# Optimization experiments

Measured on AMD Instinct MI355X. Metric: run time of the kernel, lower is better.

The kernel has to match this reference:

```python
import jax, jax.numpy as jnp
import numpy as np

B, T, D = 2, 512, 1024
H = 16
DH = D // H          # 64 head dim
E = 8                # experts
K = 2                # top-k routing
F = 4 * D            # expert hidden dim


def _layernorm(x, s, b, eps=1e-5):
    mu = jnp.mean(x, axis=-1, keepdims=True)
    var = jnp.var(x, axis=-1, keepdims=True)
    return (x - mu) * jax.lax.rsqrt(var + eps) * s + b


def setup_inputs() -> dict:
    key = jax.random.key(0)
    ks = jax.random.split(key, 16)
    sd = 0.02
    return {
        "x": jax.random.normal(ks[0], (B, T, D), jnp.float32),
        "text_state": jax.random.normal(ks[1], (B, D), jnp.float32),
        "ln1_s": jnp.ones((D,), jnp.float32),
        "ln1_b": jnp.zeros((D,), jnp.float32),
        "w_qkv": jax.random.normal(ks[2], (D, 3 * D), jnp.float32) * sd,
        "b_qkv": jnp.zeros((3 * D,), jnp.float32),
        "w_o": jax.random.normal(ks[3], (D, D), jnp.float32) * sd,
        "b_o": jnp.zeros((D,), jnp.float32),
        "rel_bias": jax.random.normal(ks[4], (H, 2 * T - 1), jnp.float32) * sd,
        "ln2_s": jnp.ones((D,), jnp.float32),
        "ln2_b": jnp.zeros((D,), jnp.float32),
        "w_txt": jax.random.normal(ks[5], (D, D), jnp.float32) * sd,
        "b_txt": jnp.zeros((D,), jnp.float32),
        "w_r": jax.random.normal(ks[6], (D, E), jnp.float32) * sd,
        "b_r": jnp.zeros((E,), jnp.float32),
        "w1": jax.random.normal(ks[7], (E, D, F), jnp.float32) * sd,
        "b1": jnp.zeros((E, F), jnp.float32),
        "w2": jax.random.normal(ks[8], (E, F, D), jnp.float32) * sd,
        "b2": jnp.zeros((E, D), jnp.float32),
    }


def reference(x, text_state, ln1_s, ln1_b, w_qkv, b_qkv, w_o, b_o, rel_bias,
              ln2_s, ln2_b, w_txt, b_txt, w_r, b_r, w1, b1, w2, b2):
    # ---- temporal-bias multi-head self-attention (pre-LN, residual) ----
    h = _layernorm(x, ln1_s, ln1_b)
    qkv = (h @ w_qkv + b_qkv).reshape(B, T, 3, H, DH)
    q, k, v = qkv[:, :, 0], qkv[:, :, 1], qkv[:, :, 2]       # [B,T,H,DH]
    scores = jnp.einsum("bthd,bshd->bhts", q, k) / np.sqrt(DH).astype(np.float32)
    idx = jnp.arange(T)
    rel = idx[None, :] - idx[:, None] + (T - 1)              # [T,T] in [0, 2T-2]
    scores = scores + rel_bias[:, rel][None]                 # broadcast [1,H,T,T]
    attn = jax.nn.softmax(scores, axis=-1)
    ctx = jnp.einsum("bhts,bshd->bthd", attn, v).reshape(B, T, D)
    x = x + ctx @ w_o + b_o

    # ---- top-k MoE feed-forward with text-conditioned router ----
    h2 = _layernorm(x, ln2_s, ln2_b)
    router_in = h2 + (text_state @ w_txt + b_txt)[:, None, :]
    probs = jax.nn.softmax(router_in @ w_r + b_r, axis=-1)   # [B,T,E]
    topv, topi = jax.lax.top_k(probs, K)                     # [B,T,K]
    gates = topv / jnp.sum(topv, axis=-1, keepdims=True)
    gates_full = jnp.einsum("btk,btke->bte", gates, jax.nn.one_hot(topi, E, dtype=x.dtype))
    # dense grouped-expert compute, sparsely combined (same math as dispatch)
    hid = jax.nn.gelu(jnp.einsum("btd,edf->btef", h2, w1) + b1)      # [B,T,E,F]
    eout = jnp.einsum("btef,efd->bted", hid, w2) + b2                # [B,T,E,D]
    y = jnp.einsum("bte,bted->btd", gates_full, eout)
    x = x + y

    diag = jnp.mean(probs, axis=(0, 1))                      # expert load [E]
    return x, diag
```

## Files before the change

kernel.cpp:

```cpp
#include <hip/hip_runtime.h>
#include <hip/hip_bf16.h>
#include <math.h>

#define BB 2
#define TT 512
#define DD 1024
#define HH 16
#define DHH 64
#define EE 8
#define FF 4096
#define NTOK 1024
#define CAP 2560
#define SPL 2

typedef __attribute__((ext_vector_type(4))) float f32x4;
typedef __attribute__((ext_vector_type(8))) short short8;

__device__ __forceinline__ short f2b(float f) {
    __hip_bfloat16 h = __float2bfloat16(f);
    return *reinterpret_cast<short*>(&h);
}
__device__ __forceinline__ float b2f(short s) {
    __hip_bfloat16 h = *reinterpret_cast<__hip_bfloat16*>(&s);
    return __bfloat162float(h);
}

__device__ __forceinline__ void gload16(const short* g, short* l) {
    __builtin_amdgcn_global_load_lds((const __attribute__((address_space(1))) unsigned int*)g,
                                     (__attribute__((address_space(3))) unsigned int*)l,
                                     16, 0, 0);
}

template <int BF>
__global__ __launch_bounds__(256) void ln_kernel(const float* __restrict__ x,
                                                 const float* __restrict__ s,
                                                 const float* __restrict__ b,
                                                 void* __restrict__ outp) {
    int row = blockIdx.x;
    int tid = threadIdx.x;
    const float* xr = x + (size_t)row * DD;
    float sm = 0.f, sq = 0.f;
    for (int i = tid; i < DD; i += 256) {
        float v = xr[i];
        sm += v; sq += v * v;
    }
    #pragma unroll
    for (int o = 32; o; o >>= 1) {
        sm += __shfl_down(sm, o);
        sq += __shfl_down(sq, o);
    }
    __shared__ float r1[4], r2[4];
    if ((tid & 63) == 0) { r1[tid >> 6] = sm; r2[tid >> 6] = sq; }
    __syncthreads();
    float tot  = r1[0] + r1[1] + r1[2] + r1[3];
    float totq = r2[0] + r2[1] + r2[2] + r2[3];
    float mu  = tot * (1.f / DD);
    float var = totq * (1.f / DD) - mu * mu;
    float inv = rsqrtf(var + 1e-5f);
    for (int i = tid; i < DD; i += 256) {
        float v = (xr[i] - mu) * inv * s[i] + b[i];
        if (BF) ((short*)outp)[(size_t)row * DD + i] = f2b(v);
        else    ((float*)outp)[(size_t)row * DD + i] = v;
    }
}

__global__ __launch_bounds__(256) void transpose_cast(const float* __restrict__ src,
                                                      short* __restrict__ dst,
                                                      int K, int N) {
    __shared__ float t[64][65];
    src += (size_t)blockIdx.z * K * N;
    dst += (size_t)blockIdx.z * K * N;
    int k0 = blockIdx.y * 64, n0 = blockIdx.x * 64;
    int rr = threadIdx.x >> 4;
    int cc = (threadIdx.x & 15) * 4;
    #pragma unroll
    for (int p = 0; p < 4; p++) {
        float4 v = *(const float4*)&src[(size_t)(k0 + rr + p * 16) * N + n0 + cc];
        t[rr + p * 16][cc]     = v.x;
        t[rr + p * 16][cc + 1] = v.y;
        t[rr + p * 16][cc + 2] = v.z;
        t[rr + p * 16][cc + 3] = v.w;
    }
    __syncthreads();
    #pragma unroll
    for (int p = 0; p < 4; p++) {
        int n = rr + p * 16;
        short4 o;
        o.x = f2b(t[cc][n]); o.y = f2b(t[cc + 1][n]);
        o.z = f2b(t[cc + 2][n]); o.w = f2b(t[cc + 3][n]);
        *(short4*)&dst[(size_t)(n0 + n) * K + k0 + cc] = o;
    }
}

__global__ __launch_bounds__(256) void v_transpose(const short* __restrict__ Vb,
                                                   short* __restrict__ VTb) {
    __shared__ short t[32][33];
    int bh = blockIdx.z;
    const short* src = Vb + (size_t)bh * TT * DHH;
    short* dst = VTb + (size_t)bh * DHH * TT;
    int t0 = blockIdx.x * 32, d0 = blockIdx.y * 32;
    int tx = threadIdx.x & 31, ty = threadIdx.x >> 5;
    #pragma unroll
    for (int p = 0; p < 4; p++)
        t[ty + p * 8][tx] = src[(size_t)(t0 + ty + p * 8) * DHH + d0 + tx];
    __syncthreads();
    #pragma unroll
    for (int p = 0; p < 4; p++)
        dst[(size_t)(d0 + ty + p * 8) * TT + t0 + tx] = t[tx][ty + p * 8];
}

__device__ __forceinline__ void gemm_loop64(const short* __restrict__ A,
                                            const short* __restrict__ B,
                                            int K, int lda, int ldb,
                                            short* As, short* Bs,
                                            f32x4 acc[2][2], int m0, int n0, int tid) {
    int wave = tid >> 6, lane = tid & 63;
    int wr = wave >> 1, wc = wave & 1;
    int lrow = lane & 15, lk = lane >> 4;
    int sr = tid >> 3, ss = tid & 7;
    int sswz = (ss ^ (sr & 7)) * 8;
    const short* Ag0 = A + (size_t)(m0 + sr) * lda + sswz;
    const short* Ag1 = A + (size_t)(m0 + sr + 32) * lda + sswz;
    const short* Bg0 = B + (size_t)(n0 + sr) * ldb + sswz;
    const short* Bg1 = B + (size_t)(n0 + sr + 32) * ldb + sswz;
    short* lA0 = As + wave * 512;
    short* lA1 = As + 2048 + wave * 512;
    short* lB0 = Bs + wave * 512;
    short* lB1 = Bs + 2048 + wave * 512;
    int nt = K >> 6;
    gload16(Ag0, lA0); gload16(Ag1, lA1);
    gload16(Bg0, lB0); gload16(Bg1, lB1);
    __syncthreads();
    for (int t = 0; t < nt; ++t) {
        int h = (t & 1) * 4096;
        if (t + 1 < nt) {
            int k0 = (t + 1) << 6;
            int hn = 4096 - h;
            gload16(Ag0 + k0, lA0 + hn); gload16(Ag1 + k0, lA1 + hn);
            gload16(Bg0 + k0, lB0 + hn); gload16(Bg1 + k0, lB1 + hn);
        }
        const uint4* Asc = (const uint4*)(As + h);
        const uint4* Bsc = (const uint4*)(Bs + h);
        #pragma unroll
        for (int kk = 0; kk < 2; kk++) {
            int slot = kk * 4 + lk;
            short8 a[2], b[2];
            #pragma unroll
            for (int i = 0; i < 2; i++) {
                int row = wr * 32 + i * 16 + lrow;
                uint4 v = Asc[row * 8 + (slot ^ (row & 7))];
                a[i] = *(short8*)&v;
            }
            #pragma unroll
            for (int j = 0; j < 2; j++) {
                int row = wc * 32 + j * 16 + lrow;
                uint4 v = Bsc[row * 8 + (slot ^ (row & 7))];
                b[j] = *(short8*)&v;
            }
            #pragma unroll
            for (int i = 0; i < 2; i++)
                #pragma unroll
                for (int j = 0; j < 2; j++)
                    acc[i][j] = __builtin_amdgcn_mfma_f32_16x16x32_bf16(a[i], b[j], acc[i][j], 0, 0, 0);
        }
        __syncthreads();
    }
}

__device__ __forceinline__ void gemm_loop_w(const short* __restrict__ A,
                                            const short* __restrict__ B,
                                            int K, short* As, short* Bs,
                                            f32x4 acc[2][4], int m0, int n0, int tid) {
    int wave = tid >> 6, lane = tid & 63;
    int wr = wave >> 1, wc = wave & 1;
    int lrow = lane & 15, lk = lane >> 4;
    int sr = tid >> 3, ss = tid & 7;
    int sswz = (ss ^ (sr & 7)) * 8;
    const short* Ag0 = A + (size_t)(m0 + sr) * K + sswz;
    const short* Ag1 = A + (size_t)(m0 + sr + 32) * K + sswz;
    const short* Bg0 = B + (size_t)(n0 + sr) * K + sswz;
    const short* Bg1 = B + (size_t)(n0 + sr + 32) * K + sswz;
    const short* Bg2 = B + (size_t)(n0 + sr + 64) * K + sswz;
    const short* Bg3 = B + (size_t)(n0 + sr + 96) * K + sswz;
    short* lA0 = As + wave * 512;
    short* lA1 = As + 2048 + wave * 512;
    short* lB0 = Bs + wave * 512;
    short* lB1 = Bs + 2048 + wave * 512;
    short* lB2 = Bs + 4096 + wave * 512;
    short* lB3 = Bs + 6144 + wave * 512;
    int nt = K >> 6;
    gload16(Ag0, lA0); gload16(Ag1, lA1);
    gload16(Bg0, lB0); gload16(Bg1, lB1);
    gload16(Bg2, lB2); gload16(Bg3, lB3);
    __syncthreads();
    for (int t = 0; t < nt; ++t) {
        int hA = (t & 1) * 4096;
        int hB = (t & 1) * 8192;
        if (t + 1 < nt) {
            int k0 = (t + 1) << 6;
            int hnA = 4096 - hA, hnB = 8192 - hB;
            gload16(Ag0 + k0, lA0 + hnA); gload16(Ag1 + k0, lA1 + hnA);
            gload16(Bg0 + k0, lB0 + hnB); gload16(Bg1 + k0, lB1 + hnB);
            gload16(Bg2 + k0, lB2 + hnB); gload16(Bg3 + k0, lB3 + hnB);
        }
        const uint4* Asc = (const uint4*)(As + hA);
        const uint4* Bsc = (const uint4*)(Bs + hB);
        #pragma unroll
        for (int kk = 0; kk < 2; kk++) {
            int slot = kk * 4 + lk;
            short8 a[2], b[4];
            #pragma unroll
            for (int i = 0; i < 2; i++) {
                int row = wr * 32 + i * 16 + lrow;
                uint4 v = Asc[row * 8 + (slot ^ (row & 7))];
                a[i] = *(short8*)&v;
            }
            #pragma unroll
            for (int j = 0; j < 4; j++) {
                int row = wc * 64 + j * 16 + lrow;
                uint4 v = Bsc[row * 8 + (slot ^ (row & 7))];
                b[j] = *(short8*)&v;
            }
            #pragma unroll
            for (int i = 0; i < 2; i++)
                #pragma unroll
                for (int j = 0; j < 4; j++)
                    acc[i][j] = __builtin_amdgcn_mfma_f32_16x16x32_bf16(a[i], b[j], acc[i][j], 0, 0, 0);
        }
        __syncthreads();
    }
}

__global__ __launch_bounds__(256) void gemm64_res_mfma(const short* __restrict__ A,
                                                       const short* __restrict__ Bw,
                                                       const float* __restrict__ bias,
                                                       const float* __restrict__ res,
                                                       float* __restrict__ C,
                                                       int N, int K) {
    __shared__ short As[8192];
    __shared__ short Bs[8192];
    int tid = threadIdx.x;
    int m0 = blockIdx.y * 64, n0 = blockIdx.x * 64;
    f32x4 acc[2][2] = {};
    gemm_loop64(A, Bw, K, K, K, As, Bs, acc, m0, n0, tid);
    int wave = tid >> 6, lane = tid & 63;
    int wr = wave >> 1, wc = wave & 1;
    int lrow = lane & 15, lk = lane >> 4;
    #pragma unroll
    for (int i = 0; i < 2; i++) {
        #pragma unroll
        for (int j = 0; j < 2; j++) {
            int col = n0 + wc * 32 + j * 16 + lrow;
            float bv = bias[col];
            #pragma unroll
            for (int r = 0; r < 4; r++) {
                int row = m0 + wr * 32 + i * 16 + lk * 4 + r;
                C[(size_t)row * N + col] = acc[i][j][r] + bv + res[(size_t)row * N + col];
            }
        }
    }
}

__global__ __launch_bounds__(256) void qkv_mfma(const short* __restrict__ A,
                                                const short* __restrict__ Bw,
                                                const float* __restrict__ bias,
                                                short* __restrict__ Qb,
                                                short* __restrict__ Kb,
                                                short* __restrict__ Vb) {
    __shared__ short As[8192];
    __shared__ short Bs[16384];
    int tid = threadIdx.x;
    int m0 = blockIdx.y * 64, n0 = blockIdx.x * 128;
    f32x4 acc[2][4] = {};
    gemm_loop_w(A, Bw, DD, As, Bs, acc, m0, n0, tid);
    int wave = tid >> 6, lane = tid & 63;
    int wr = wave >> 1, wc = wave & 1;
    int lrow = lane & 15, lk = lane >> 4;
    #pragma unroll
    for (int i = 0; i < 2; i++) {
        #pragma unroll
        for (int j = 0; j < 4; j++) {
            int col = n0 + wc * 64 + j * 16 + lrow;
            int part = col >> 10;
            int rem = col & 1023;
            int h = rem >> 6, d = rem & 63;
            short* dst = (part == 0) ? Qb : ((part == 1) ? Kb : Vb);
            float bv = bias[col];
            #pragma unroll
            for (int r = 0; r < 4; r++) {
                int row = m0 + wr * 32 + i * 16 + lk * 4 + r;
                int b = row >> 9, t = row & (TT - 1);
                dst[(((size_t)(b * HH + h)) * TT + t) * DHH + d] = f2b(acc[i][j][r] + bv);
            }
        }
    }
}

__global__ __launch_bounds__(256) void scores_mfma(const short* __restrict__ Qb,
                                                   const short* __restrict__ Kb,
                                                   float* __restrict__ S) {
    __shared__ short As[8192];
    __shared__ short Bs[16384];
    int tid = threadIdx.x;
    int bh = blockIdx.z;
    const short* A = Qb + (size_t)bh * TT * DHH;
    const short* B = Kb + (size_t)bh * TT * DHH;
    float* Sp = S + (size_t)bh * TT * TT;
    int m0 = blockIdx.y * 64, n0 = blockIdx.x * 128;
    f32x4 acc[2][4] = {};
    gemm_loop_w(A, B, DHH, As, Bs, acc, m0, n0, tid);
    int wave = tid >> 6, lane = tid & 63;
    int wr = wave >> 1, wc = wave & 1;
    int lrow = lane & 15, lk = lane >> 4;
    #pragma unroll
    for (int i = 0; i < 2; i++)
        #pragma unroll
        for (int j = 0; j < 4; j++) {
            int col = n0 + wc * 64 + j * 16 + lrow;
            #pragma unroll
            for (int r = 0; r < 4; r++) {
                int row = m0 + wr * 32 + i * 16 + lk * 4 + r;
                Sp[(size_t)row * TT + col] = acc[i][j][r];
            }
        }
}

__global__ __launch_bounds__(256) void softmax_kernel(const float* __restrict__ S,
                                                      const float* __restrict__ rel_bias,
                                                      short* __restrict__ P) {
    int row = blockIdx.x * 4 + (threadIdx.x >> 6);
    int lane = threadIdx.x & 63;
    int t = row & (TT - 1), h = (row >> 9) & (HH - 1);
    const float* Sr = S + (size_t)row * TT;
    const float* br = rel_bias + h * (2 * TT - 1) + (TT - 1) - t;
    float v[8];
    float mx = -1e30f;
    #pragma unroll
    for (int i = 0; i < 8; i++) {
        int s = lane + i * 64;
        v[i] = Sr[s] * 0.125f + br[s];
        mx = fmaxf(mx, v[i]);
    }
    #pragma unroll
    for (int o = 32; o; o >>= 1) mx = fmaxf(mx, __shfl_xor(mx, o));
    float sum = 0.f;
    #pragma unroll
    for (int i = 0; i < 8; i++) { v[i] = expf(v[i] - mx); sum += v[i]; }
    #pragma unroll
    for (int o = 32; o; o >>= 1) sum += __shfl_xor(sum, o);
    float inv = 1.f / sum;
    #pragma unroll
    for (int i = 0; i < 8; i++)
        P[(size_t)row * TT + lane + i * 64] = f2b(v[i] * inv);
}

__global__ __launch_bounds__(256) void pv_mfma(const short* __restrict__ P,
                                               const short* __restrict__ VTb,
                                               short* __restrict__ ctxb) {
    __shared__ short As[8192];
    __shared__ short Bs[8192];
    int tid = threadIdx.x;
    int bh = blockIdx.z;
    int h = bh & (HH - 1), b = bh >> 4;
    const short* A = P + (size_t)bh * TT * TT;
    const short* B = VTb + (size_t)bh * DHH * TT;
    int m0 = blockIdx.y * 64;
    f32x4 acc[2][2] = {};
    gemm_loop64(A, B, TT, TT, TT, As, Bs, acc, m0, 0, tid);
    int wave = tid >> 6, lane = tid & 63;
    int wr = wave >> 1, wc = wave & 1;
    int lrow = lane & 15, lk = lane >> 4;
    #pragma unroll
    for (int i = 0; i < 2; i++)
        #pragma unroll
        for (int j = 0; j < 2; j++) {
            int d = wc * 32 + j * 16 + lrow;
            #pragma unroll
            for (int r = 0; r < 4; r++) {
                int row = m0 + wr * 32 + i * 16 + lk * 4 + r;
                ctxb[((size_t)(b * TT + row)) * DD + h * DHH + d] = f2b(acc[i][j][r]);
            }
        }
}

__global__ __launch_bounds__(256) void moe_gemm1_mfma(const short* __restrict__ Ag,
                                                      const short* __restrict__ W1t,
                                                      const float* __restrict__ b1,
                                                      const int* __restrict__ counts,
                                                      const int* __restrict__ offs,
                                                      short* __restrict__ hid) {
    int e = blockIdx.y >> 5, tile = blockIdx.y & 31;
    int cnt = counts[e];
    int pcnt = (cnt + 63) & ~63;
    int row0 = tile * 64;
    if (row0 >= pcnt) return;
    int base = offs[e];
    const short* A  = Ag + (size_t)base * DD;
    const short* Bw = W1t + (size_t)e * FF * DD;
    __shared__ short As[8192];
    __shared__ short Bs[16384];
    int tid = threadIdx.x;
    int n0 = blockIdx.x * 128;
    f32x4 acc[2][4] = {};
    gemm_loop_w(A, Bw, DD, As, Bs, acc, row0, n0, tid);
    int wave = tid >> 6, lane = tid & 63;
    int wr = wave >> 1, wc = wave & 1;
    int lrow = lane & 15, lk = lane >> 4;
    #pragma unroll
    for (int i = 0; i < 2; i++) {
        #pragma unroll
        for (int j = 0; j < 4; j++) {
            int col = n0 + wc * 64 + j * 16 + lrow;
            float bv = b1[e * FF + col];
            #pragma unroll
            for (int r = 0; r < 4; r++) {
                int row = row0 + wr * 32 + i * 16 + lk * 4 + r;
                float v = acc[i][j][r] + bv;
                float u = 0.7978845608028654f * (v + 0.044715f * v * v * v);
                float g = 0.5f * v * (1.f + tanhf(u));
                hid[(size_t)(base + row) * FF + col] = f2b(g);
            }
        }
    }
}

__global__ __launch_bounds__(256) void moe_gemm2_mfma(const short* __restrict__ hid,
                                                      const short* __restrict__ W2t,
                                                      const float* __restrict__ b2,
                                                      const float* __restrict__ pair_gate,
                                                      const int* __restrict__ counts,
                                                      const int* __restrict__ offs,
                                                      short* __restrict__ pair_part) {
    int s = blockIdx.z;
    int e = blockIdx.y >> 5, tile = blockIdx.y & 31;
    int cnt = counts[e];
    int pcnt = (cnt + 63) & ~63;
    int row0 = tile * 64;
    if (row0 >= pcnt) return;
    int base = offs[e];
    const int KS = FF / SPL;
    const short* A  = hid + (size_t)base * FF + s * KS;
    const short* Bw = W2t + (size_t)e * DD * FF + s * KS;
    __shared__ short As[8192];
    __shared__ short Bs[8192];
    int tid = threadIdx.x;
    int n0 = blockIdx.x * 64;
    f32x4 acc[2][2] = {};
    gemm_loop64(A, Bw, KS, FF, FF, As, Bs, acc, row0, n0, tid);
    int wave = tid >> 6, lane = tid & 63;
    int wr = wave >> 1, wc = wave & 1;
    int lrow = lane & 15, lk = lane >> 4;
    #pragma unroll
    for (int i = 0; i < 2; i++) {
        #pragma unroll
        for (int j = 0; j < 2; j++) {
            int col = n0 + wc * 32 + j * 16 + lrow;
            float bv = (s == 0) ? b2[e * DD + col] : 0.f;
            #pragma unroll
            for (int r = 0; r < 4; r++) {
                int row = row0 + wr * 32 + i * 16 + lk * 4 + r;
                float g = pair_gate[base + row];
                pair_part[((size_t)s * CAP + base + row) * DD + col] = f2b(g * (acc[i][j][r] + bv));
            }
        }
    }
}

__global__ __launch_bounds__(256) void txt_kernel(const float* __restrict__ ts,
                                                  const float* __restrict__ w,
                                                  const float* __restrict__ bias,
                                                  float* __restrict__ out) {
    int gid = blockIdx.x * 256 + threadIdx.x;
    int b = gid >> 10;
    int n = gid & (DD - 1);
    float acc = 0.f;
    for (int d = 0; d < DD; d++) acc += ts[b * DD + d] * w[(size_t)d * DD + n];
    out[gid] = acc + bias[n];
}

__global__ __launch_bounds__(256) void router_kernel(const float* __restrict__ h2,
                                                     const float* __restrict__ txt,
                                                     const float* __restrict__ w_r,
                                                     const float* __restrict__ b_r,
                                                     float* __restrict__ probs,
                                                     float* __restrict__ gates,
                                                     int* __restrict__ counts) {
    int row = blockIdx.x;
    int b = row >> 9;
    int tid = threadIdx.x;
    float acc[EE] = {};
    for (int d = tid; d < DD; d += 256) {
        float r = h2[(size_t)row * DD + d] + txt[b * DD + d];
        #pragma unroll
        for (int e = 0; e < EE; e++) acc[e] += r * w_r[d * EE + e];
    }
    #pragma unroll
    for (int e = 0; e < EE; e++)
        #pragma unroll
        for (int o = 32; o; o >>= 1) acc[e] += __shfl_down(acc[e], o);
    __shared__ float lds[4][EE];
    int lane = tid & 63, w = tid >> 6;
    if (lane == 0)
        for (int e = 0; e < EE; e++) lds[w][e] = acc[e];
    __syncthreads();
    if (tid == 0) {
        float lg[EE], p[EE];
        float mx = -1e30f;
        for (int e = 0; e < EE; e++) {
            lg[e] = lds[0][e] + lds[1][e] + lds[2][e] + lds[3][e] + b_r[e];
            mx = fmaxf(mx, lg[e]);
        }
        float sum = 0.f;
        for (int e = 0; e < EE; e++) { p[e] = expf(lg[e] - mx); sum += p[e]; }
        float invs = 1.f / sum;
        for (int e = 0; e < EE; e++) { p[e] *= invs; probs[row * EE + e] = p[e]; }
        int i1 = 0;
        for (int e = 1; e < EE; e++) if (p[e] > p[i1]) i1 = e;
        int i2 = (i1 == 0) ? 1 : 0;
        for (int e = 0; e < EE; e++) if (e != i1 && p[e] > p[i2]) i2 = e;
        float gs = p[i1] + p[i2];
        for (int e = 0; e < EE; e++) gates[row * EE + e] = 0.f;
        gates[row * EE + i1] = p[i1] / gs;
        gates[row * EE + i2] = p[i2] / gs;
        atomicAdd(&counts[i1], 1);
        atomicAdd(&counts[i2], 1);
    }
}

__global__ void offs_kernel(const int* __restrict__ counts, int* __restrict__ offs) {
    if (threadIdx.x == 0) {
        int acc = 0;
        for (int e = 0; e < EE; e++) { offs[e] = acc; acc += (counts[e] + 63) & ~63; }
    }
}

__global__ __launch_bounds__(256) void scatter_kernel(const float* __restrict__ gates,
                                                      const int* __restrict__ offs,
                                                      int* __restrict__ fill,
                                                      int* __restrict__ tok_pos,
                                                      float* __restrict__ pair_gate) {
    int t = blockIdx.x * 256 + threadIdx.x;
    if (t >= NTOK) return;
    int slot = 0;
    for (int e = 0; e < EE; e++) {
        float g = gates[t * EE + e];
        if (g > 0.f) {
            int pos = offs[e] + atomicAdd(&fill[e], 1);
            tok_pos[t * 2 + slot] = pos;
            pair_gate[pos] = g;
            slot++;
        }
    }
}

__global__ __launch_bounds__(256) void gather_tokens(const float* __restrict__ h2,
                                                     const int* __restrict__ tok_pos,
                                                     short* __restrict__ Ag) {
    int i = blockIdx.x;
    int pos = tok_pos[i];
    int t = i >> 1;
    int d = threadIdx.x * 4;
    #pragma unroll
    for (int k = 0; k < 4; k++)
        Ag[(size_t)pos * DD + d + k] = f2b(h2[(size_t)t * DD + d + k]);
}

__global__ __launch_bounds__(256) void diag_kernel(const float* __restrict__ probs,
                                                   float* __restrict__ out) {
    int e = blockIdx.x;
    int tid = threadIdx.x;
    float s = 0.f;
    for (int t = tid; t < NTOK; t += 256) s += probs[t * EE + e];
    #pragma unroll
    for (int o = 32; o; o >>= 1) s += __shfl_down(s, o);
    __shared__ float red[4];
    if ((tid & 63) == 0) red[tid >> 6] = s;
    __syncthreads();
    if (tid == 0) out[e] = (red[0] + red[1] + red[2] + red[3]) * (1.f / NTOK);
}

__global__ __launch_bounds__(256) void finaladd_kernel(float* __restrict__ out,
                                                       const short* __restrict__ pair_part,
                                                       const int* __restrict__ tok_pos) {
    int t = blockIdx.x;
    int d = threadIdx.x * 4;
    float4 a = *(const float4*)&out[(size_t)t * DD + d];
    #pragma unroll
    for (int sl = 0; sl < 2; sl++) {
        int pos = tok_pos[2 * t + sl];
        #pragma unroll
        for (int s = 0; s < SPL; s++) {
            short4 v = *(const short4*)&pair_part[((size_t)s * CAP + pos) * DD + d];
            a.x += b2f(v.x); a.y += b2f(v.y); a.z += b2f(v.z); a.w += b2f(v.w);
        }
    }
    *(float4*)&out[(size_t)t * DD + d] = a;
}

extern "C" void kernel_launch(void* const* d_in, const int* in_sizes, int n_in,
                              void* d_out, int out_size, void* d_ws, size_t ws_size,
                              hipStream_t stream) {
    const float* x          = (const float*)d_in[0];
    const float* text_state = (const float*)d_in[1];
    const float* ln1_s      = (const float*)d_in[2];
    const float* ln1_b      = (const float*)d_in[3];
    const float* w_qkv      = (const float*)d_in[4];
    const float* b_qkv      = (const float*)d_in[5];
    const float* w_o        = (const float*)d_in[6];
    const float* b_o        = (const float*)d_in[7];
    const float* rel_bias   = (const float*)d_in[8];
    const float* ln2_s      = (const float*)d_in[9];
    const float* ln2_b      = (const float*)d_in[10];
    const float* w_txt      = (const float*)d_in[11];
    const float* b_txt      = (const float*)d_in[12];
    const float* w_r        = (const float*)d_in[13];
    const float* b_r        = (const float*)d_in[14];
    const float* w1         = (const float*)d_in[15];
    const float* b1         = (const float*)d_in[16];
    const float* w2         = (const float*)d_in[17];
    const float* b2         = (const float*)d_in[18];

    float* out = (float*)d_out;

    char* p = (char*)d_ws;
    auto alloc = [&](size_t bytes) { char* r = p; p += (bytes + 255) & ~(size_t)255; return r; };
    short* h1b      = (short*)alloc((size_t)NTOK * DD * 2);
    short* Qb       = (short*)alloc((size_t)NTOK * DD * 2);
    short* Kb       = (short*)alloc((size_t)NTOK * DD * 2);
    short* Vb       = (short*)alloc((size_t)NTOK * DD * 2);
    short* VTb      = (short*)alloc((size_t)NTOK * DD * 2);
    char*  region1  = alloc((size_t)BB * HH * TT * TT * 4);
    char*  region2  = alloc((size_t)BB * HH * TT * TT * 2);
    short* ctxb     = (short*)alloc((size_t)NTOK * DD * 2);
    float* h2       = (float*)alloc((size_t)NTOK * DD * 4);
    float* txt      = (float*)alloc((size_t)BB * DD * 4);
    float* probs    = (float*)alloc((size_t)NTOK * EE * 4);
    float* gates    = (float*)alloc((size_t)NTOK * EE * 4);
    float* pair_gate= (float*)alloc((size_t)CAP * 4);
    int*   counts   = (int*)alloc(8 * 4);
    int*   fill     = (int*)alloc(8 * 4);
    int*   offs     = (int*)alloc(8 * 4);
    int*   tok_pos  = (int*)alloc((size_t)NTOK * 2 * 4);
    short* wqkvT    = (short*)alloc((size_t)3 * DD * DD * 2);
    short* woT      = (short*)alloc((size_t)DD * DD * 2);
    short* w1T      = (short*)alloc((size_t)EE * FF * DD * 2);
    short* w2T      = (short*)alloc((size_t)EE * DD * FF * 2);

    float* S         = (float*)region1;
    short* P         = (short*)region2;
    short* Ag        = (short*)region1;
    short* hid       = (short*)(region1 + (((size_t)CAP * DD * 2 + 255) & ~(size_t)255));
    short* pair_part = (short*)region2;

    transpose_cast<<<dim3(3 * DD / 64, DD / 64, 1), 256, 0, stream>>>(w_qkv, wqkvT, DD, 3 * DD);
    transpose_cast<<<dim3(DD / 64, DD / 64, 1), 256, 0, stream>>>(w_o, woT, DD, DD);
    transpose_cast<<<dim3(FF / 64, DD / 64, EE), 256, 0, stream>>>(w1, w1T, DD, FF);
    transpose_cast<<<dim3(DD / 64, FF / 64, EE), 256, 0, stream>>>(w2, w2T, FF, DD);

    ln_kernel<1><<<NTOK, 256, 0, stream>>>(x, ln1_s, ln1_b, h1b);
    qkv_mfma<<<dim3(3 * DD / 128, NTOK / 64), 256, 0, stream>>>(h1b, wqkvT, b_qkv, Qb, Kb, Vb);
    v_transpose<<<dim3(TT / 32, DHH / 32, BB * HH), 256, 0, stream>>>(Vb, VTb);
    scores_mfma<<<dim3(TT / 128, TT / 64, BB * HH), 256, 0, stream>>>(Qb, Kb, S);
    softmax_kernel<<<BB * HH * TT / 4, 256, 0, stream>>>(S, rel_bias, P);
    pv_mfma<<<dim3(1, TT / 64, BB * HH), 256, 0, stream>>>(P, VTb, ctxb);
    gemm64_res_mfma<<<dim3(DD / 64, NTOK / 64), 256, 0, stream>>>(ctxb, woT, b_o, x, out, DD, DD);
    ln_kernel<0><<<NTOK, 256, 0, stream>>>(out, ln2_s, ln2_b, h2);
    txt_kernel<<<(BB * DD) / 256, 256, 0, stream>>>(text_state, w_txt, b_txt, txt);
    hipMemsetAsync(counts, 0, 8 * 4, stream);
    hipMemsetAsync(fill, 0, 8 * 4, stream);
    hipMemsetAsync(Ag, 0, (size_t)CAP * DD * 2, stream);
    router_kernel<<<NTOK, 256, 0, stream>>>(h2, txt, w_r, b_r, probs, gates, counts);
    offs_kernel<<<1, 64, 0, stream>>>(counts, offs);
    scatter_kernel<<<NTOK / 256, 256, 0, stream>>>(gates, offs, fill, tok_pos, pair_gate);
    gather_tokens<<<NTOK * 2, 256, 0, stream>>>(h2, tok_pos, Ag);
    diag_kernel<<<EE, 256, 0, stream>>>(probs, out + (size_t)NTOK * DD);
    moe_gemm1_mfma<<<dim3(FF / 128, EE * 32), 256, 0, stream>>>(Ag, w1T, b1, counts, offs, hid);
    moe_gemm2_mfma<<<dim3(DD / 64, EE * 32, SPL), 256, 0, stream>>>(hid, w2T, b2, pair_gate, counts, offs, pair_part);
    finaladd_kernel<<<NTOK, 256, 0, stream>>>(out, pair_part, tok_pos);
}
```

Baseline: 408.2 us.

## Use 128x128 MFMA tiles for MoE GEMMs and parallelize text projection reduction

```diff
diff --git a/kernel.cpp b/kernel.cpp
--- a/kernel.cpp
+++ b/kernel.cpp
@@ -10,7 +10,7 @@
 #define EE 8
 #define FF 4096
 #define NTOK 1024
-#define CAP 2560
+#define CAP 3072
 #define SPL 2
 
 typedef __attribute__((ext_vector_type(4))) float f32x4;
@@ -107,6 +107,52 @@
     #pragma unroll
     for (int p = 0; p < 4; p++)
         dst[(size_t)(d0 + ty + p * 8) * TT + t0 + tx] = t[tx][ty + p * 8];
+}
+
+__device__ __forceinline__ void gemm_loop128(const short* __restrict__ A,
+                                             const short* __restrict__ B,
+                                             int K, int lda, int ldb,
+                                             short* As, short* Bs,
+                                             f32x4 acc[4][4], int m0, int n0, int tid) {
+    int wave = tid >> 6, lane = tid & 63;
+    int wr = wave >> 1, wc = wave & 1;
+    int lrow = lane & 15, lk = lane >> 4;
+    int srow = lane >> 3;
+    int sslot = (lane & 7) ^ srow;
+    const short* Agb = A + (size_t)(m0 + srow) * lda + sslot * 8;
+    const short* Bgb = B + (size_t)(n0 + srow) * ldb + sslot * 8;
+    for (int k0 = 0; k0 < K; k0 += 64) {
+        #pragma unroll
+        for (int p = 0; p < 4; p++) {
+            int rg = (wave * 4 + p) * 8;
+            gload16(Agb + (size_t)rg * lda + k0, As + rg * 64);
+            gload16(Bgb + (size_t)rg * ldb + k0, Bs + rg * 64);
+        }
+        __syncthreads();
+        #pragma unroll
+        for (int kk = 0; kk < 2; kk++) {
+            int q = kk * 4 + lk;
+            short8 a[4], b[4];
+            #pragma unroll
+            for (int i = 0; i < 4; i++) {
+                int r = wr * 64 + i * 16 + lrow;
+                uint4 v = ((const uint4*)As)[r * 8 + (q ^ (r & 7))];
+                a[i] = *(short8*)&v;
+            }
+            #pragma unroll
+            for (int j = 0; j < 4; j++) {
+                int r = wc * 64 + j * 16 + lrow;
+                uint4 v = ((const uint4*)Bs)[r * 8 + (q ^ (r & 7))];
+                b[j] = *(short8*)&v;
+            }
+            #pragma unroll
+            for (int i = 0; i < 4; i++)
+                #pragma unroll
+                for (int j = 0; j < 4; j++)
+                    acc[i][j] = __builtin_amdgcn_mfma_f32_16x16x32_bf16(a[i], b[j], acc[i][j], 0, 0, 0);
+        }
+        __syncthreads();
+    }
 }
 
 __device__ __forceinline__ void gemm_loop64(const short* __restrict__ A,
@@ -389,32 +435,32 @@
                                                       const int* __restrict__ counts,
                                                       const int* __restrict__ offs,
                                                       short* __restrict__ hid) {
-    int e = blockIdx.y >> 5, tile = blockIdx.y & 31;
+    int e = blockIdx.y >> 4, tile = blockIdx.y & 15;
     int cnt = counts[e];
-    int pcnt = (cnt + 63) & ~63;
-    int row0 = tile * 64;
+    int pcnt = (cnt + 127) & ~127;
+    int row0 = tile * 128;
     if (row0 >= pcnt) return;
     int base = offs[e];
     const short* A  = Ag + (size_t)base * DD;
     const short* Bw = W1t + (size_t)e * FF * DD;
     __shared__ short As[8192];
-    __shared__ short Bs[16384];
+    __shared__ short Bs[8192];
     int tid = threadIdx.x;
     int n0 = blockIdx.x * 128;
-    f32x4 acc[2][4] = {};
-    gemm_loop_w(A, Bw, DD, As, Bs, acc, row0, n0, tid);
-    int wave = tid >> 6, lane = tid & 63;
-    int wr = wave >> 1, wc = wave & 1;
-    int lrow = lane & 15, lk = lane >> 4;
-    #pragma unroll
-    for (int i = 0; i < 2; i++) {
+    f32x4 acc[4][4] = {};
+    gemm_loop128(A, Bw, DD, DD, DD, As, Bs, acc, row0, n0, tid);
+    int wave = tid >> 6, lane = tid & 63;
+    int wr = wave >> 1, wc = wave & 1;
+    int lrow = lane & 15, lk = lane >> 4;
+    #pragma unroll
+    for (int i = 0; i < 4; i++) {
         #pragma unroll
         for (int j = 0; j < 4; j++) {
             int col = n0 + wc * 64 + j * 16 + lrow;
             float bv = b1[e * FF + col];
             #pragma unroll
             for (int r = 0; r < 4; r++) {
-                int row = row0 + wr * 32 + i * 16 + lk * 4 + r;
+                int row = row0 + wr * 64 + i * 16 + lk * 4 + r;
                 float v = acc[i][j][r] + bv;
                 float u = 0.7978845608028654f * (v + 0.044715f * v * v * v);
                 float g = 0.5f * v * (1.f + tanhf(u));
@@ -432,10 +478,10 @@
                                                       const int* __restrict__ offs,
                                                       short* __restrict__ pair_part) {
     int s = blockIdx.z;
-    int e = blockIdx.y >> 5, tile = blockIdx.y & 31;
+    int e = blockIdx.y >> 4, tile = blockIdx.y & 15;
     int cnt = counts[e];
-    int pcnt = (cnt + 63) & ~63;
-    int row0 = tile * 64;
+    int pcnt = (cnt + 127) & ~127;
+    int row0 = tile * 128;
     if (row0 >= pcnt) return;
     int base = offs[e];
     const int KS = FF / SPL;
@@ -444,21 +490,21 @@
     __shared__ short As[8192];
     __shared__ short Bs[8192];
     int tid = threadIdx.x;
-    int n0 = blockIdx.x * 64;
-    f32x4 acc[2][2] = {};
-    gemm_loop64(A, Bw, KS, FF, FF, As, Bs, acc, row0, n0, tid);
-    int wave = tid >> 6, lane = tid & 63;
-    int wr = wave >> 1, wc = wave & 1;
-    int lrow = lane & 15, lk = lane >> 4;
-    #pragma unroll
-    for (int i = 0; i < 2; i++) {
-        #pragma unroll
-        for (int j = 0; j < 2; j++) {
-            int col = n0 + wc * 32 + j * 16 + lrow;
+    int n0 = blockIdx.x * 128;
+    f32x4 acc[4][4] = {};
+    gemm_loop128(A, Bw, KS, FF, FF, As, Bs, acc, row0, n0, tid);
+    int wave = tid >> 6, lane = tid & 63;
+    int wr = wave >> 1, wc = wave & 1;
+    int lrow = lane & 15, lk = lane >> 4;
+    #pragma unroll
+    for (int i = 0; i < 4; i++) {
+        #pragma unroll
+        for (int j = 0; j < 4; j++) {
+            int col = n0 + wc * 64 + j * 16 + lrow;
             float bv = (s == 0) ? b2[e * DD + col] : 0.f;
             #pragma unroll
             for (int r = 0; r < 4; r++) {
-                int row = row0 + wr * 32 + i * 16 + lk * 4 + r;
+                int row = row0 + wr * 64 + i * 16 + lk * 4 + r;
                 float g = pair_gate[base + row];
                 pair_part[((size_t)s * CAP + base + row) * DD + col] = f2b(g * (acc[i][j][r] + bv));
             }
@@ -470,12 +516,21 @@
                                                   const float* __restrict__ w,
                                                   const float* __restrict__ bias,
                                                   float* __restrict__ out) {
-    int gid = blockIdx.x * 256 + threadIdx.x;
-    int b = gid >> 10;
-    int n = gid & (DD - 1);
+    int b = blockIdx.y;
+    int col = blockIdx.x * 32 + (threadIdx.x & 31);
+    int dg = threadIdx.x >> 5;
     float acc = 0.f;
-    for (int d = 0; d < DD; d++) acc += ts[b * DD + d] * w[(size_t)d * DD + n];
-    out[gid] = acc + bias[n];
+    for (int d = dg * 128; d < dg * 128 + 128; d++)
+        acc += ts[b * DD + d] * w[(size_t)d * DD + col];
+    __shared__ float red[8][32];
+    red[dg][threadIdx.x & 31] = acc;
+    __syncthreads();
+    if (threadIdx.x < 32) {
+        float s = 0.f;
+        #pragma unroll
+        for (int g = 0; g < 8; g++) s += red[g][threadIdx.x];
+        out[b * DD + col] = s + bias[col];
+    }
 }
 
 __global__ __launch_bounds__(256) void router_kernel(const float* __restrict__ h2,
@@ -530,7 +585,7 @@
 __global__ void offs_kernel(const int* __restrict__ counts, int* __restrict__ offs) {
     if (threadIdx.x == 0) {
         int acc = 0;
-        for (int e = 0; e < EE; e++) { offs[e] = acc; acc += (counts[e] + 63) & ~63; }
+        for (int e = 0; e < EE; e++) { offs[e] = acc; acc += (counts[e] + 127) & ~127; }
     }
 }
 
@@ -665,7 +720,7 @@
     pv_mfma<<<dim3(1, TT / 64, BB * HH), 256, 0, stream>>>(P, VTb, ctxb);
     gemm64_res_mfma<<<dim3(DD / 64, NTOK / 64), 256, 0, stream>>>(ctxb, woT, b_o, x, out, DD, DD);
     ln_kernel<0><<<NTOK, 256, 0, stream>>>(out, ln2_s, ln2_b, h2);
-    txt_kernel<<<(BB * DD) / 256, 256, 0, stream>>>(text_state, w_txt, b_txt, txt);
+    txt_kernel<<<dim3(DD / 32, BB), 256, 0, stream>>>(text_state, w_txt, b_txt, txt);
     hipMemsetAsync(counts, 0, 8 * 4, stream);
     hipMemsetAsync(fill, 0, 8 * 4, stream);
     hipMemsetAsync(Ag, 0, (size_t)CAP * DD * 2, stream);
@@ -674,7 +729,7 @@
     scatter_kernel<<<NTOK / 256, 256, 0, stream>>>(gates, offs, fill, tok_pos, pair_gate);
     gather_tokens<<<NTOK * 2, 256, 0, stream>>>(h2, tok_pos, Ag);
     diag_kernel<<<EE, 256, 0, stream>>>(probs, out + (size_t)NTOK * DD);
-    moe_gemm1_mfma<<<dim3(FF / 128, EE * 32), 256, 0, stream>>>(Ag, w1T, b1, counts, offs, hid);
-    moe_gemm2_mfma<<<dim3(DD / 64, EE * 32, SPL), 256, 0, stream>>>(hid, w2T, b2, pair_gate, counts, offs, pair_part);
+    moe_gemm1_mfma<<<dim3(FF / 128, EE * 16), 256, 0, stream>>>(Ag, w1T, b1, counts, offs, hid);
+    moe_gemm2_mfma<<<dim3(DD / 128, EE * 16, SPL), 256, 0, stream>>>(hid, w2T, b2, pair_gate, counts, offs, pair_part);
     finaladd_kernel<<<NTOK, 256, 0, stream>>>(out, pair_part, tok_pos);
 }
```

New measurement: 335.9 us (median of 2 runs). 17.7% less time.
